# Optimization experiments

Hardware: AMD Instinct MI355X
Metric: run time of the kernel (lower is better)

Reference implementation:

```python
import jax, jax.numpy as jnp
import numpy as np

N_NODES = 50000
N_EDGES = 1600000
IN_CH = 128
OUT_CH = 64
HEADS = 2
NEG_SLOPE = 0.2


def setup_inputs() -> dict:
    key = jax.random.key(0)
    ks = jax.random.split(key, 9)
    return {
        "x": jax.random.normal(ks[0], (N_NODES, IN_CH), dtype=jnp.float32),
        "embedding": jax.random.normal(ks[1], (N_NODES, OUT_CH), dtype=jnp.float32),
        "lin_w": jax.random.normal(ks[2], (IN_CH, HEADS * OUT_CH), dtype=jnp.float32) * (1.0 / np.sqrt(IN_CH)),
        "att_i": jax.random.normal(ks[3], (HEADS, OUT_CH), dtype=jnp.float32) * 0.1,
        "att_j": jax.random.normal(ks[4], (HEADS, OUT_CH), dtype=jnp.float32) * 0.1,
        "att_em_i": jax.random.normal(ks[5], (HEADS, OUT_CH), dtype=jnp.float32) * 0.1,
        "att_em_j": jax.random.normal(ks[6], (HEADS, OUT_CH), dtype=jnp.float32) * 0.1,
        "edge_src": jax.random.randint(ks[7], (N_EDGES,), 0, N_NODES, dtype=jnp.int64 if jax.config.read("jax_enable_x64") else jnp.int32),
        "edge_dst": jax.random.randint(ks[8], (N_EDGES,), 0, N_NODES, dtype=jnp.int64 if jax.config.read("jax_enable_x64") else jnp.int32),
    }


def reference(x, embedding, lin_w, att_i, att_j, att_em_i, att_em_j, edge_src, edge_dst):
    N = x.shape[0]
    H, D = att_i.shape
    # linear projection: [N, H, D]
    xh = (x @ lin_w).reshape(N, H, D)
    # add self loops
    loop = jnp.arange(N, dtype=edge_src.dtype)
    src = jnp.concatenate([edge_src, loop])
    dst = jnp.concatenate([edge_dst, loop])
    # per-node attention scores (cat(x, emb) . cat(att, att_em) split into two dots)
    s_i = jnp.einsum("nhd,hd->nh", xh, att_i) + embedding @ att_em_i.T  # [N,H]
    s_j = jnp.einsum("nhd,hd->nh", xh, att_j) + embedding @ att_em_j.T  # [N,H]
    # per-edge attention: x_i is src feature, x_j is dst feature (as in source)
    alpha = jax.nn.leaky_relu(s_i[src] + s_j[dst], negative_slope=NEG_SLOPE)  # [E+N,H]
    alpha = jax.nn.softmax(alpha, axis=1)  # softmax over heads, per the source code
    # message is alpha * x[dst]; aggregated at dst => x[n] * sum of alpha over incoming edges
    w = jax.ops.segment_sum(alpha, dst, num_segments=N)  # [N,H]
    out = xh * w[:, :, None]  # [N,H,D]
    return out.mean(axis=1)  # [N,D]
```

## Files before the change

kernel.cpp:

```cpp
#include <hip/hip_runtime.h>

#define IN_CH 128
#define OUT_CH 64
#define NEG_SLOPE 0.2f

#define CHUNK 2048
#define BSHIFT 10
#define NGEMM 391
#define CAPMAX 36864
#define FIX22 4194304.0f

typedef short bf16x8 __attribute__((ext_vector_type(8)));
typedef float f32x4 __attribute__((ext_vector_type(4)));
typedef unsigned long long u64;
typedef unsigned int u32;

__device__ __forceinline__ unsigned short f2bf(float f) {
  union { float f; unsigned u; } v;
  v.f = f;
  unsigned r = v.u + 0x7FFF + ((v.u >> 16) & 1);
  return (unsigned short)(r >> 16);
}

__device__ __forceinline__ float bf2f(unsigned short h) {
  union { unsigned u; float f; } v;
  v.u = (unsigned)h << 16;
  return v.f;
}

__global__ __launch_bounds__(256) void prep_kernel(
    const float* __restrict__ lw, const float* __restrict__ att_i,
    const float* __restrict__ att_j, unsigned short* __restrict__ lwt,
    float* __restrict__ u, int* __restrict__ gcur) {
  const int bid = blockIdx.x;
  const int tid = threadIdx.x;
  if (bid == 0) gcur[tid] = 0;
  if (bid < 64) {
    int idx = bid * 256 + tid;
    int k = idx >> 7;
    int c = idx & 127;
    lwt[(size_t)c * IN_CH + k] = f2bf(lw[idx]);
  } else {
    int which = bid - 64;
    const float* att = which ? att_j : att_i;
    int k = tid & 127;
    int h = (tid >> 7) & 1;
    float v = 0.f;
#pragma unroll 8
    for (int d = 0; d < 64; ++d)
      v = fmaf(lw[(size_t)k * IN_CH + h * 64 + d], att[h * 64 + d], v);
    u[which * 256 + h * 128 + k] = v;
  }
}

__global__ __launch_bounds__(256) void score_kernel(
    const float* __restrict__ x, const float* __restrict__ emb,
    const float* __restrict__ u, const float* __restrict__ aei,
    const float* __restrict__ aej, float2* __restrict__ si,
    float2* __restrict__ sj, float* __restrict__ wself,
    u64* __restrict__ wsum64, int N) {
  const int tid = threadIdx.x;
  const int wave = tid >> 6;
  const int lane = tid & 63;
  const int n = blockIdx.x * 4 + wave;
  if (n >= N) return;

  float x0 = x[(size_t)n * IN_CH + lane];
  float x1 = x[(size_t)n * IN_CH + 64 + lane];
  float em = emb[(size_t)n * OUT_CH + lane];

  float v_si0 = fmaf(x0, u[lane], fmaf(x1, u[64 + lane], em * aei[lane]));
  float v_si1 =
      fmaf(x0, u[128 + lane], fmaf(x1, u[192 + lane], em * aei[64 + lane]));
  float v_sj0 =
      fmaf(x0, u[256 + lane], fmaf(x1, u[320 + lane], em * aej[lane]));
  float v_sj1 =
      fmaf(x0, u[384 + lane], fmaf(x1, u[448 + lane], em * aej[64 + lane]));

#pragma unroll
  for (int off = 32; off > 0; off >>= 1) {
    v_si0 += __shfl_xor(v_si0, off, 64);
    v_si1 += __shfl_xor(v_si1, off, 64);
    v_sj0 += __shfl_xor(v_sj0, off, 64);
    v_sj1 += __shfl_xor(v_sj1, off, 64);
  }

  if (lane == 0) {
    si[n] = make_float2(v_si0, v_si1);
    sj[n] = make_float2(v_sj0, v_sj1);
    float a0 = v_si0 + v_sj0;
    float a1 = v_si1 + v_sj1;
    a0 = a0 > 0.f ? a0 : NEG_SLOPE * a0;
    a1 = a1 > 0.f ? a1 : NEG_SLOPE * a1;
    wself[n] = 1.f / (1.f + __expf(a1 - a0));
    wsum64[n] = 0ull;
  }
}

__global__ __launch_bounds__(256) void bin_gemm_kernel(
    const float* __restrict__ x, const unsigned short* __restrict__ lwt,
    const int* __restrict__ esrc, const int* __restrict__ edst,
    const float2* __restrict__ si, const float2* __restrict__ sj,
    unsigned short* __restrict__ xhb, u64* __restrict__ wsum64,
    u32* __restrict__ brecs, int* __restrict__ gcur, int cap, int nbin, int N,
    int E) {
  __shared__ u32 recs[CHUNK];
  __shared__ int hist[64];
  __shared__ int scan[64];
  __shared__ int gbase[64];
  __shared__ int cur[64];
  const int bid = blockIdx.x;
  const int tid = threadIdx.x;
  const int wave = tid >> 6;
  const int lane = tid & 63;

  if (bid < nbin) {
    if (tid < 64) hist[tid] = 0;
    __syncthreads();

    const long e0 = (long)bid * CHUNK;
    const int cnt = (int)min((long)CHUNK, (long)E - e0);

    for (int r = tid; r < cnt; r += 256)
      atomicAdd(&hist[edst[e0 + r] >> BSHIFT], 1);
    __syncthreads();

    if (tid < 64) {
      int h = hist[tid];
      int v = h;
#pragma unroll
      for (int off = 1; off < 64; off <<= 1) {
        int t = __shfl_up(v, off, 64);
        if (tid >= off) v += t;
      }
      int excl = v - h;
      scan[tid] = excl;
      cur[tid] = excl;
      gbase[tid] = (h > 0) ? atomicAdd(&gcur[tid], h) : 0;
    }
    __syncthreads();

    for (int r = tid; r < cnt; r += 256) {
      long e = e0 + r;
      int s = esrc[e];
      int d = edst[e];
      float2 aa = si[s];
      float2 bb = sj[d];
      float a0 = aa.x + bb.x;
      float a1 = aa.y + bb.y;
      a0 = a0 > 0.f ? a0 : NEG_SLOPE * a0;
      a1 = a1 > 0.f ? a1 : NEG_SLOPE * a1;
      float p0 = 1.f / (1.f + __expf(a1 - a0));
      u32 fx = (u32)fminf(p0 * FIX22 + 0.5f, 4194303.0f);
      int pos = atomicAdd(&cur[d >> BSHIFT], 1);
      recs[pos] = ((u32)(d & 1023) << 22) | fx;
    }
    __syncthreads();

    for (int p = tid; p < cnt; p += 256) {
      int lo = 0, hi = 63;
#pragma unroll
      for (int it = 0; it < 6; ++it) {
        int mid = (lo + hi + 1) >> 1;
        if (scan[mid] <= p) lo = mid; else hi = mid - 1;
      }
      int b = lo;
      int gofs = gbase[b] + (p - scan[b]);
      u32 rec = recs[p];
      if (gofs < cap) {
        brecs[(size_t)b * cap + gofs] = rec;
      } else {
        atomicAdd(&wsum64[(b << BSHIFT) + (int)(rec >> 22)],
                  (1ull << 32) | (u64)(rec & 0x3FFFFFu));
      }
    }
  } else {
    const int g = bid - nbin;
    const int ntiles = (N + 63) / 64;
    const int ko = (lane >> 4) * 8;
    const int ccol = lane & 15;
    for (int tile = g; tile < ntiles; tile += NGEMM) {
      const int row0 = tile * 64 + wave * 16;
      int arow = row0 + (lane & 15);
      if (arow >= N) arow = N - 1;
      const float* ap = x + (size_t)arow * IN_CH + ko;
      bf16x8 a[4];
#pragma unroll
      for (int kb = 0; kb < 4; ++kb) {
        float4 f0 = *(const float4*)(ap + kb * 32);
        float4 f1 = *(const float4*)(ap + kb * 32 + 4);
        bf16x8 t;
        t[0] = (short)f2bf(f0.x); t[1] = (short)f2bf(f0.y);
        t[2] = (short)f2bf(f0.z); t[3] = (short)f2bf(f0.w);
        t[4] = (short)f2bf(f1.x); t[5] = (short)f2bf(f1.y);
        t[6] = (short)f2bf(f1.z); t[7] = (short)f2bf(f1.w);
        a[kb] = t;
      }
      const int crow0 = row0 + (lane >> 4) * 4;
#pragma unroll
      for (int nt = 0; nt < 8; ++nt) {
        f32x4 acc = {0.f, 0.f, 0.f, 0.f};
        const bf16x8* bp =
            (const bf16x8*)(lwt + (size_t)(nt * 16 + ccol) * IN_CH + ko);
        acc = __builtin_amdgcn_mfma_f32_16x16x32_bf16(a[0], bp[0], acc, 0, 0, 0);
        acc = __builtin_amdgcn_mfma_f32_16x16x32_bf16(a[1], bp[4], acc, 0, 0, 0);
        acc = __builtin_amdgcn_mfma_f32_16x16x32_bf16(a[2], bp[8], acc, 0, 0, 0);
        acc = __builtin_amdgcn_mfma_f32_16x16x32_bf16(a[3], bp[12], acc, 0, 0, 0);
#pragma unroll
        for (int rr = 0; rr < 4; ++rr) {
          int n = crow0 + rr;
          if (n < N) xhb[(size_t)n * IN_CH + nt * 16 + ccol] = f2bf(acc[rr]);
        }
      }
    }
  }
}

__global__ __launch_bounds__(1024) void reduce_out_kernel(
    const unsigned short* __restrict__ xhb, const u64* __restrict__ wsum64,
    const float* __restrict__ wself, const u32* __restrict__ brecs,
    const int* __restrict__ gcur, int cap, float* __restrict__ out, int N) {
  __shared__ u64 tab[256];
  const int bid = blockIdx.x;
  const int p = bid >> 2;
  const int q = bid & 3;
  const int tid = threadIdx.x;

  if (tid < 256) tab[tid] = 0ull;
  __syncthreads();

  const int cnt = min(gcur[p], cap);
  const u32* rp = brecs + (size_t)p * cap;
  for (int r = tid; r < cnt; r += 1024) {
    u32 rec = rp[r];
    if ((int)(rec >> 30) == q)
      atomicAdd(&tab[(rec >> 22) & 255], (1ull << 32) | (u64)(rec & 0x3FFFFFu));
  }
  __syncthreads();

  const int n0 = (p << BSHIFT) + (q << 8);
  const int nmax = min(256, N - n0);
  if (nmax <= 0) return;
  for (int t = tid; t < nmax * 16; t += 1024) {
    int ln = t >> 4;
    int n = n0 + ln;
    int c4 = (t & 15) << 2;
    u64 acc = tab[ln] + wsum64[n];
    float cnt_f = (float)(u32)(acc >> 32);
    float s0 = (float)(u32)(acc & 0xFFFFFFFFu) * (1.0f / FIX22);
    float ps = wself[n];
    float w0 = 0.5f * (s0 + ps);
    float w1 = 0.5f * ((cnt_f - s0) + (1.f - ps));
    ushort4 h0 = *(const ushort4*)&xhb[(size_t)n * IN_CH + c4];
    ushort4 h1 = *(const ushort4*)&xhb[(size_t)n * IN_CH + 64 + c4];
    float4 o;
    o.x = fmaf(bf2f(h0.x), w0, bf2f(h1.x) * w1);
    o.y = fmaf(bf2f(h0.y), w0, bf2f(h1.y) * w1);
    o.z = fmaf(bf2f(h0.z), w0, bf2f(h1.z) * w1);
    o.w = fmaf(bf2f(h0.w), w0, bf2f(h1.w) * w1);
    *(float4*)&out[(size_t)n * OUT_CH + c4] = o;
  }
}

extern "C" void kernel_launch(void* const* d_in, const int* in_sizes, int n_in,
                              void* d_out, int out_size, void* d_ws,
                              size_t ws_size, hipStream_t stream) {
  const float* x = (const float*)d_in[0];
  const float* emb = (const float*)d_in[1];
  const float* lw = (const float*)d_in[2];
  const float* att_i = (const float*)d_in[3];
  const float* att_j = (const float*)d_in[4];
  const float* aei = (const float*)d_in[5];
  const float* aej = (const float*)d_in[6];
  const int* esrc = (const int*)d_in[7];
  const int* edst = (const int*)d_in[8];
  float* out = (float*)d_out;

  int N = in_sizes[0] / IN_CH;
  int E = in_sizes[7];
  int nbkt = (N + 1023) >> BSHIFT;
  int nbin = (E + CHUNK - 1) / CHUNK;

  char* ws = (char*)d_ws;
  u64* wsum64 = (u64*)ws;
  float2* si = (float2*)(wsum64 + N);
  float2* sj = si + N;
  float* wself = (float*)(sj + N);
  float* u = wself + N;
  unsigned short* lwt = (unsigned short*)(u + 512);
  unsigned short* xhb = lwt + 16384;
  int* gcur = (int*)(xhb + (size_t)N * IN_CH);
  u32* brecs = (u32*)(gcur + 256);

  size_t fixed = (size_t)((char*)brecs - ws);
  size_t avail = ws_size > fixed ? (ws_size - fixed) / 4 : 0;
  int cap = (int)(avail / (nbkt > 0 ? nbkt : 1));
  if (cap > CAPMAX) cap = CAPMAX;
  if (cap < 4096) cap = 4096;

  prep_kernel<<<dim3(66), dim3(256), 0, stream>>>(lw, att_i, att_j, lwt, u,
                                                  gcur);
  score_kernel<<<dim3((N + 3) / 4), dim3(256), 0, stream>>>(
      x, emb, u, aei, aej, si, sj, wself, wsum64, N);
  bin_gemm_kernel<<<dim3(nbin + NGEMM), dim3(256), 0, stream>>>(
      x, lwt, esrc, edst, si, sj, xhb, wsum64, brecs, gcur, cap, nbin, N, E);
  reduce_out_kernel<<<dim3(nbkt * 4), dim3(1024), 0, stream>>>(
      xhb, wsum64, wself, brecs, gcur, cap, out, N);
}
```

Before: 171.5 us.

## Fuse all four stages into one persistent cooperative kernel with grid syncs

Merges the prep, score, bin/GEMM and reduce kernels into a single cooperative persistent kernel that uses grid.sync between phases, removing three kernel launches and their inter-kernel gaps. The binning phase now processes larger chunks with edge loads batched into registers so more gathers are in flight, and the grid is sized from occupancy with a fixed 3:1 bin/GEMM split. The reduce phase runs with 256 threads per block instead of 1024. Risks include grid-sync overhead, lower parallelism in the prep, reduce and GEMM phases, and a hardcoded 256-CU assumption in the grid size.

```diff
diff --git a/kernel.cpp b/kernel.cpp
--- a/kernel.cpp
+++ b/kernel.cpp
@@ -1,12 +1,14 @@
 #include <hip/hip_runtime.h>
+#include <hip/hip_cooperative_groups.h>
+
+namespace cg = cooperative_groups;
 
 #define IN_CH 128
 #define OUT_CH 64
 #define NEG_SLOPE 0.2f
 
-#define CHUNK 2048
 #define BSHIFT 10
-#define NGEMM 391
+#define CEDGE 2304
 #define CAPMAX 36864
 #define FIX22 4194304.0f
 
@@ -28,158 +30,173 @@
   return v.f;
 }
 
-__global__ __launch_bounds__(256) void prep_kernel(
+__global__ __launch_bounds__(256, 4) void fused_kernel(
+    const float* __restrict__ x, const float* __restrict__ emb,
     const float* __restrict__ lw, const float* __restrict__ att_i,
-    const float* __restrict__ att_j, unsigned short* __restrict__ lwt,
-    float* __restrict__ u, int* __restrict__ gcur) {
-  const int bid = blockIdx.x;
-  const int tid = threadIdx.x;
-  if (bid == 0) gcur[tid] = 0;
-  if (bid < 64) {
-    int idx = bid * 256 + tid;
-    int k = idx >> 7;
-    int c = idx & 127;
-    lwt[(size_t)c * IN_CH + k] = f2bf(lw[idx]);
-  } else {
-    int which = bid - 64;
-    const float* att = which ? att_j : att_i;
-    int k = tid & 127;
-    int h = (tid >> 7) & 1;
-    float v = 0.f;
-#pragma unroll 8
-    for (int d = 0; d < 64; ++d)
-      v = fmaf(lw[(size_t)k * IN_CH + h * 64 + d], att[h * 64 + d], v);
-    u[which * 256 + h * 128 + k] = v;
-  }
-}
-
-__global__ __launch_bounds__(256) void score_kernel(
-    const float* __restrict__ x, const float* __restrict__ emb,
-    const float* __restrict__ u, const float* __restrict__ aei,
-    const float* __restrict__ aej, float2* __restrict__ si,
+    const float* __restrict__ att_j, const float* __restrict__ aei,
+    const float* __restrict__ aej, const int* __restrict__ esrc,
+    const int* __restrict__ edst, float* __restrict__ out,
+    u64* __restrict__ wsum64, float2* __restrict__ si,
     float2* __restrict__ sj, float* __restrict__ wself,
-    u64* __restrict__ wsum64, int N) {
-  const int tid = threadIdx.x;
-  const int wave = tid >> 6;
-  const int lane = tid & 63;
-  const int n = blockIdx.x * 4 + wave;
-  if (n >= N) return;
-
-  float x0 = x[(size_t)n * IN_CH + lane];
-  float x1 = x[(size_t)n * IN_CH + 64 + lane];
-  float em = emb[(size_t)n * OUT_CH + lane];
-
-  float v_si0 = fmaf(x0, u[lane], fmaf(x1, u[64 + lane], em * aei[lane]));
-  float v_si1 =
-      fmaf(x0, u[128 + lane], fmaf(x1, u[192 + lane], em * aei[64 + lane]));
-  float v_sj0 =
-      fmaf(x0, u[256 + lane], fmaf(x1, u[320 + lane], em * aej[lane]));
-  float v_sj1 =
-      fmaf(x0, u[384 + lane], fmaf(x1, u[448 + lane], em * aej[64 + lane]));
-
-#pragma unroll
-  for (int off = 32; off > 0; off >>= 1) {
-    v_si0 += __shfl_xor(v_si0, off, 64);
-    v_si1 += __shfl_xor(v_si1, off, 64);
-    v_sj0 += __shfl_xor(v_sj0, off, 64);
-    v_sj1 += __shfl_xor(v_sj1, off, 64);
-  }
-
-  if (lane == 0) {
-    si[n] = make_float2(v_si0, v_si1);
-    sj[n] = make_float2(v_sj0, v_sj1);
-    float a0 = v_si0 + v_sj0;
-    float a1 = v_si1 + v_sj1;
-    a0 = a0 > 0.f ? a0 : NEG_SLOPE * a0;
-    a1 = a1 > 0.f ? a1 : NEG_SLOPE * a1;
-    wself[n] = 1.f / (1.f + __expf(a1 - a0));
-    wsum64[n] = 0ull;
-  }
-}
-
-__global__ __launch_bounds__(256) void bin_gemm_kernel(
-    const float* __restrict__ x, const unsigned short* __restrict__ lwt,
-    const int* __restrict__ esrc, const int* __restrict__ edst,
-    const float2* __restrict__ si, const float2* __restrict__ sj,
-    unsigned short* __restrict__ xhb, u64* __restrict__ wsum64,
-    u32* __restrict__ brecs, int* __restrict__ gcur, int cap, int nbin, int N,
-    int E) {
-  __shared__ u32 recs[CHUNK];
-  __shared__ int hist[64];
-  __shared__ int scan[64];
-  __shared__ int gbase[64];
-  __shared__ int cur[64];
+    float* __restrict__ u, unsigned short* __restrict__ lwt,
+    unsigned short* __restrict__ xhb, int* __restrict__ gcur,
+    u32* __restrict__ brecs, int cap, int N, int E, int nbin, int nchunk,
+    int nred) {
+  cg::grid_group grid = cg::this_grid();
+  __shared__ u32 recs[CEDGE];
+  __shared__ int hist[64], scn[64], gbase[64], cur[64];
+  __shared__ u64 tab[256];
+
+  const int G = gridDim.x;
   const int bid = blockIdx.x;
   const int tid = threadIdx.x;
   const int wave = tid >> 6;
   const int lane = tid & 63;
 
-  if (bid < nbin) {
-    if (tid < 64) hist[tid] = 0;
-    __syncthreads();
-
-    const long e0 = (long)bid * CHUNK;
-    const int cnt = (int)min((long)CHUNK, (long)E - e0);
-
-    for (int r = tid; r < cnt; r += 256)
-      atomicAdd(&hist[edst[e0 + r] >> BSHIFT], 1);
-    __syncthreads();
-
-    if (tid < 64) {
-      int h = hist[tid];
-      int v = h;
-#pragma unroll
-      for (int off = 1; off < 64; off <<= 1) {
-        int t = __shfl_up(v, off, 64);
-        if (tid >= off) v += t;
-      }
-      int excl = v - h;
-      scan[tid] = excl;
-      cur[tid] = excl;
-      gbase[tid] = (h > 0) ? atomicAdd(&gcur[tid], h) : 0;
-    }
-    __syncthreads();
-
-    for (int r = tid; r < cnt; r += 256) {
-      long e = e0 + r;
-      int s = esrc[e];
-      int d = edst[e];
-      float2 aa = si[s];
-      float2 bb = sj[d];
-      float a0 = aa.x + bb.x;
-      float a1 = aa.y + bb.y;
+  for (int vb = bid; vb < 66; vb += G) {
+    if (vb < 64) {
+      int idx = vb * 256 + tid;
+      int k = idx >> 7;
+      int c = idx & 127;
+      lwt[(size_t)c * IN_CH + k] = f2bf(lw[idx]);
+    } else {
+      int which = vb - 64;
+      const float* att = which ? att_j : att_i;
+      int k = tid & 127;
+      int h = (tid >> 7) & 1;
+      float v = 0.f;
+#pragma unroll 8
+      for (int d = 0; d < 64; ++d)
+        v = fmaf(lw[(size_t)k * IN_CH + h * 64 + d], att[h * 64 + d], v);
+      u[which * 256 + h * 128 + k] = v;
+    }
+  }
+  if (bid == 0) gcur[tid] = 0;
+  grid.sync();
+
+  for (int n = bid * 4 + wave; n < N; n += G * 4) {
+    float x0 = x[(size_t)n * IN_CH + lane];
+    float x1 = x[(size_t)n * IN_CH + 64 + lane];
+    float em = emb[(size_t)n * OUT_CH + lane];
+
+    float v_si0 = fmaf(x0, u[lane], fmaf(x1, u[64 + lane], em * aei[lane]));
+    float v_si1 =
+        fmaf(x0, u[128 + lane], fmaf(x1, u[192 + lane], em * aei[64 + lane]));
+    float v_sj0 =
+        fmaf(x0, u[256 + lane], fmaf(x1, u[320 + lane], em * aej[lane]));
+    float v_sj1 =
+        fmaf(x0, u[384 + lane], fmaf(x1, u[448 + lane], em * aej[64 + lane]));
+
+#pragma unroll
+    for (int off = 32; off > 0; off >>= 1) {
+      v_si0 += __shfl_xor(v_si0, off, 64);
+      v_si1 += __shfl_xor(v_si1, off, 64);
+      v_sj0 += __shfl_xor(v_sj0, off, 64);
+      v_sj1 += __shfl_xor(v_sj1, off, 64);
+    }
+
+    if (lane == 0) {
+      si[n] = make_float2(v_si0, v_si1);
+      sj[n] = make_float2(v_sj0, v_sj1);
+      float a0 = v_si0 + v_sj0;
+      float a1 = v_si1 + v_sj1;
       a0 = a0 > 0.f ? a0 : NEG_SLOPE * a0;
       a1 = a1 > 0.f ? a1 : NEG_SLOPE * a1;
-      float p0 = 1.f / (1.f + __expf(a1 - a0));
-      u32 fx = (u32)fminf(p0 * FIX22 + 0.5f, 4194303.0f);
-      int pos = atomicAdd(&cur[d >> BSHIFT], 1);
-      recs[pos] = ((u32)(d & 1023) << 22) | fx;
-    }
-    __syncthreads();
-
-    for (int p = tid; p < cnt; p += 256) {
-      int lo = 0, hi = 63;
-#pragma unroll
-      for (int it = 0; it < 6; ++it) {
-        int mid = (lo + hi + 1) >> 1;
-        if (scan[mid] <= p) lo = mid; else hi = mid - 1;
-      }
-      int b = lo;
-      int gofs = gbase[b] + (p - scan[b]);
-      u32 rec = recs[p];
-      if (gofs < cap) {
-        brecs[(size_t)b * cap + gofs] = rec;
-      } else {
-        atomicAdd(&wsum64[(b << BSHIFT) + (int)(rec >> 22)],
-                  (1ull << 32) | (u64)(rec & 0x3FFFFFu));
-      }
+      wself[n] = 1.f / (1.f + __expf(a1 - a0));
+      wsum64[n] = 0ull;
+    }
+  }
+  grid.sync();
+
+  if (bid < nbin) {
+    for (int c = bid; c < nchunk; c += nbin) {
+      const long e0 = (long)c * CEDGE;
+      const int cnt = (int)min((long)CEDGE, (long)E - e0);
+      const int kcnt = (cnt + 255) >> 8;
+
+      if (tid < 64) hist[tid] = 0;
+      __syncthreads();
+
+      int dv[9];
+#pragma unroll
+      for (int k = 0; k < 9; ++k) {
+        long e = e0 + (k << 8) + tid;
+        dv[k] = (k < kcnt && e < E) ? edst[e] : -1;
+      }
+#pragma unroll
+      for (int k = 0; k < 9; ++k)
+        if (dv[k] >= 0) atomicAdd(&hist[dv[k] >> BSHIFT], 1);
+      __syncthreads();
+
+      if (tid < 64) {
+        int h = hist[tid];
+        int v = h;
+#pragma unroll
+        for (int off = 1; off < 64; off <<= 1) {
+          int t = __shfl_up(v, off, 64);
+          if (tid >= off) v += t;
+        }
+        int excl = v - h;
+        scn[tid] = excl;
+        cur[tid] = excl;
+        gbase[tid] = (h > 0) ? atomicAdd(&gcur[tid], h) : 0;
+      }
+      __syncthreads();
+
+      float2 av[9], bv[9];
+#pragma unroll
+      for (int k = 0; k < 9; ++k) {
+        if (dv[k] >= 0) {
+          long e = e0 + (k << 8) + tid;
+          av[k] = si[esrc[e]];
+          bv[k] = sj[dv[k]];
+        }
+      }
+#pragma unroll
+      for (int k = 0; k < 9; ++k) {
+        if (dv[k] >= 0) {
+          float a0 = av[k].x + bv[k].x;
+          float a1 = av[k].y + bv[k].y;
+          a0 = a0 > 0.f ? a0 : NEG_SLOPE * a0;
+          a1 = a1 > 0.f ? a1 : NEG_SLOPE * a1;
+          float p0 = 1.f / (1.f + __expf(a1 - a0));
+          u32 fx = (u32)fminf(p0 * FIX22 + 0.5f, 4194303.0f);
+          int pos = atomicAdd(&cur[dv[k] >> BSHIFT], 1);
+          recs[pos] = ((u32)(dv[k] & 1023) << 22) | fx;
+        }
+      }
+      __syncthreads();
+
+#pragma unroll
+      for (int k = 0; k < 9; ++k) {
+        int p = (k << 8) + tid;
+        if (k < kcnt && p < cnt) {
+          int lo = 0, hi = 63;
+#pragma unroll
+          for (int it = 0; it < 6; ++it) {
+            int mid = (lo + hi + 1) >> 1;
+            if (scn[mid] <= p) lo = mid; else hi = mid - 1;
+          }
+          int b = lo;
+          int gofs = gbase[b] + (p - scn[b]);
+          u32 rec = recs[p];
+          if (gofs < cap) {
+            brecs[(size_t)b * cap + gofs] = rec;
+          } else {
+            atomicAdd(&wsum64[(b << BSHIFT) + (int)(rec >> 22)],
+                      (1ull << 32) | (u64)(rec & 0x3FFFFFu));
+          }
+        }
+      }
+      __syncthreads();
     }
   } else {
     const int g = bid - nbin;
+    const int ngemm = G - nbin;
     const int ntiles = (N + 63) / 64;
     const int ko = (lane >> 4) * 8;
     const int ccol = lane & 15;
-    for (int tile = g; tile < ntiles; tile += NGEMM) {
+    for (int tile = g; tile < ntiles; tile += ngemm) {
       const int row0 = tile * 64 + wave * 16;
       int arow = row0 + (lane & 15);
       if (arow >= N) arow = N - 1;
@@ -214,51 +231,49 @@
       }
     }
   }
-}
-
-__global__ __launch_bounds__(1024) void reduce_out_kernel(
-    const unsigned short* __restrict__ xhb, const u64* __restrict__ wsum64,
-    const float* __restrict__ wself, const u32* __restrict__ brecs,
-    const int* __restrict__ gcur, int cap, float* __restrict__ out, int N) {
-  __shared__ u64 tab[256];
-  const int bid = blockIdx.x;
-  const int p = bid >> 2;
-  const int q = bid & 3;
-  const int tid = threadIdx.x;
-
-  if (tid < 256) tab[tid] = 0ull;
-  __syncthreads();
-
-  const int cnt = min(gcur[p], cap);
-  const u32* rp = brecs + (size_t)p * cap;
-  for (int r = tid; r < cnt; r += 1024) {
-    u32 rec = rp[r];
-    if ((int)(rec >> 30) == q)
-      atomicAdd(&tab[(rec >> 22) & 255], (1ull << 32) | (u64)(rec & 0x3FFFFFu));
-  }
-  __syncthreads();
-
-  const int n0 = (p << BSHIFT) + (q << 8);
-  const int nmax = min(256, N - n0);
-  if (nmax <= 0) return;
-  for (int t = tid; t < nmax * 16; t += 1024) {
-    int ln = t >> 4;
-    int n = n0 + ln;
-    int c4 = (t & 15) << 2;
-    u64 acc = tab[ln] + wsum64[n];
-    float cnt_f = (float)(u32)(acc >> 32);
-    float s0 = (float)(u32)(acc & 0xFFFFFFFFu) * (1.0f / FIX22);
-    float ps = wself[n];
-    float w0 = 0.5f * (s0 + ps);
-    float w1 = 0.5f * ((cnt_f - s0) + (1.f - ps));
-    ushort4 h0 = *(const ushort4*)&xhb[(size_t)n * IN_CH + c4];
-    ushort4 h1 = *(const ushort4*)&xhb[(size_t)n * IN_CH + 64 + c4];
-    float4 o;
-    o.x = fmaf(bf2f(h0.x), w0, bf2f(h1.x) * w1);
-    o.y = fmaf(bf2f(h0.y), w0, bf2f(h1.y) * w1);
-    o.z = fmaf(bf2f(h0.z), w0, bf2f(h1.z) * w1);
-    o.w = fmaf(bf2f(h0.w), w0, bf2f(h1.w) * w1);
-    *(float4*)&out[(size_t)n * OUT_CH + c4] = o;
+  grid.sync();
+
+  for (int m = bid; m < nred; m += G) {
+    const int p = m >> 2;
+    const int q = m & 3;
+    tab[tid] = 0ull;
+    __syncthreads();
+
+    const int cnt = min(gcur[p], cap);
+    const u32* rp = brecs + (size_t)p * cap;
+#pragma unroll 4
+    for (int r = tid; r < cnt; r += 256) {
+      u32 rec = rp[r];
+      if ((int)(rec >> 30) == q)
+        atomicAdd(&tab[(rec >> 22) & 255],
+                  (1ull << 32) | (u64)(rec & 0x3FFFFFu));
+    }
+    __syncthreads();
+
+    const int n0 = (p << BSHIFT) + (q << 8);
+    const int nmax = min(256, N - n0);
+    if (nmax > 0) {
+      for (int t = tid; t < nmax * 16; t += 256) {
+        int ln = t >> 4;
+        int n = n0 + ln;
+        int c4 = (t & 15) << 2;
+        u64 acc = tab[ln] + wsum64[n];
+        float cnt_f = (float)(u32)(acc >> 32);
+        float s0 = (float)(u32)(acc & 0xFFFFFFFFu) * (1.0f / FIX22);
+        float ps = wself[n];
+        float w0 = 0.5f * (s0 + ps);
+        float w1 = 0.5f * ((cnt_f - s0) + (1.f - ps));
+        ushort4 h0 = *(const ushort4*)&xhb[(size_t)n * IN_CH + c4];
+        ushort4 h1 = *(const ushort4*)&xhb[(size_t)n * IN_CH + 64 + c4];
+        float4 o;
+        o.x = fmaf(bf2f(h0.x), w0, bf2f(h1.x) * w1);
+        o.y = fmaf(bf2f(h0.y), w0, bf2f(h1.y) * w1);
+        o.z = fmaf(bf2f(h0.z), w0, bf2f(h1.z) * w1);
+        o.w = fmaf(bf2f(h0.w), w0, bf2f(h1.w) * w1);
+        *(float4*)&out[(size_t)n * OUT_CH + c4] = o;
+      }
+    }
+    __syncthreads();
   }
 }
 
@@ -279,7 +294,8 @@
   int N = in_sizes[0] / IN_CH;
   int E = in_sizes[7];
   int nbkt = (N + 1023) >> BSHIFT;
-  int nbin = (E + CHUNK - 1) / CHUNK;
+  int nchunk = (E + CEDGE - 1) / CEDGE;
+  int nred = nbkt * 4;
 
   char* ws = (char*)d_ws;
   u64* wsum64 = (u64*)ws;
@@ -298,12 +314,26 @@
   if (cap > CAPMAX) cap = CAPMAX;
   if (cap < 4096) cap = 4096;
 
-  prep_kernel<<<dim3(66), dim3(256), 0, stream>>>(lw, att_i, att_j, lwt, u,
-                                                  gcur);
-  score_kernel<<<dim3((N + 3) / 4), dim3(256), 0, stream>>>(
-      x, emb, u, aei, aej, si, sj, wself, wsum64, N);
-  bin_gemm_kernel<<<dim3(nbin + NGEMM), dim3(256), 0, stream>>>(
-      x, lwt, esrc, edst, si, sj, xhb, wsum64, brecs, gcur, cap, nbin, N, E);
-  reduce_out_kernel<<<dim3(nbkt * 4), dim3(1024), 0, stream>>>(
-      xhb, wsum64, wself, brecs, gcur, cap, out, N);
+  static int bpc = 0;
+  if (bpc == 0) {
+    int nb = 0;
+    hipError_t err =
+        hipOccupancyMaxActiveBlocksPerMultiprocessor(&nb, fused_kernel, 256, 0);
+    if (err != hipSuccess || nb <= 0) nb = 4;
+    bpc = nb > 4 ? 4 : nb;
+  }
+  int G = 256 * bpc;
+  int nbin = (G * 3) >> 2;
+
+  void* args[] = {(void*)&x,     (void*)&emb,    (void*)&lw,
+                  (void*)&att_i, (void*)&att_j,  (void*)&aei,
+                  (void*)&aej,   (void*)&esrc,   (void*)&edst,
+                  (void*)&out,   (void*)&wsum64, (void*)&si,
+                  (void*)&sj,    (void*)&wself,  (void*)&u,
+                  (void*)&lwt,   (void*)&xhb,    (void*)&gcur,
+                  (void*)&brecs, (void*)&cap,    (void*)&N,
+                  (void*)&E,     (void*)&nbin,   (void*)&nchunk,
+                  (void*)&nred};
+  hipLaunchCooperativeKernel((void*)fused_kernel, dim3(G), dim3(256), args, 0,
+                             stream);
 }
```

New measurement: 387.0 us. 126% more time.
